# Performance work log

Hardware: AMD Instinct MI355X
Metric: run time of the kernel (lower is better)

The kernel has to match this reference:

```python
import jax, jax.numpy as jnp
import numpy as np

N_NODES = 50000
N_EDGES = 800000
D_FEAT = 128
HIDDEN = 256
N_CLASSES = 2


def setup_inputs() -> dict:
    key = jax.random.key(0)
    ks = jax.random.split(key, 9)
    x = jax.random.normal(ks[0], (N_NODES, D_FEAT), dtype=jnp.float32)
    edge_index = jax.random.randint(ks[1], (2, N_EDGES), 0, N_NODES, dtype=jnp.int32)
    # SAGEConv params: lin_l (applied to aggregated neighbors), lin_r (root), bias
    s1 = 1.0 / np.sqrt(D_FEAT)
    s2 = 1.0 / np.sqrt(HIDDEN)
    W1l = jax.random.normal(ks[2], (D_FEAT, HIDDEN), dtype=jnp.float32) * s1
    W1r = jax.random.normal(ks[3], (D_FEAT, HIDDEN), dtype=jnp.float32) * s1
    b1 = jax.random.normal(ks[4], (HIDDEN,), dtype=jnp.float32) * s1
    W2l = jax.random.normal(ks[5], (HIDDEN, N_CLASSES), dtype=jnp.float32) * s2
    W2r = jax.random.normal(ks[6], (HIDDEN, N_CLASSES), dtype=jnp.float32) * s2
    b2 = jax.random.normal(ks[7], (N_CLASSES,), dtype=jnp.float32) * s2
    return {"x": x, "edge_index": edge_index, "W1l": W1l, "W1r": W1r,
            "b1": b1, "W2l": W2l, "W2r": W2r, "b2": b2}


def _sage_conv(x, src, dst, Wl, Wr, b):
    # mean-aggregate neighbor features x[src] into destination nodes
    n = x.shape[0]
    agg = jax.ops.segment_sum(x[src], dst, num_segments=n)  # [N, d]
    deg = jax.ops.segment_sum(jnp.ones((src.shape[0],), x.dtype), dst,
                              num_segments=n)
    mean = agg / jnp.maximum(deg, 1.0)[:, None]
    return mean @ Wl + x @ Wr + b


def reference(x, edge_index, W1l, W1r, b1, W2l, W2r, b2):
    src, dst = edge_index[0], edge_index[1]
    h = jax.nn.relu(_sage_conv(x, src, dst, W1l, W1r, b1))
    embeddings = h  # dropout is identity in eval mode
    out = jax.nn.sigmoid(_sage_conv(embeddings, src, dst, W2l, W2r, b2))
    return out, embeddings
```

## Files before the change

kernel.cpp:

```cpp
#include <hip/hip_runtime.h>
#include <math.h>

#define N_NODES 50000
#define N_EDGES 800000
#define D_FEAT 128
#define HIDDEN 256
#define NB_SCAN 196
#define GEMM_BLOCKS 1563

#define AGG_B 2048

#define CVT_B 512
#define CNT_B 3125
#define CP_B (CVT_B + CNT_B)
#define SCAT_B 3125

typedef __bf16 bf16x8 __attribute__((ext_vector_type(8)));
typedef float f32x4 __attribute__((ext_vector_type(4)));

__device__ __forceinline__ unsigned f2b(float f) {
    unsigned u = __builtin_bit_cast(unsigned, f);
    return (u + 0x7fff + ((u >> 16) & 1)) >> 16;
}

__global__ __launch_bounds__(256) void count_prep(
    const float* __restrict__ x, const int* __restrict__ dst,
    const float* __restrict__ W1l, const float* __restrict__ W1r,
    int* __restrict__ cnt, unsigned short* __restrict__ rank,
    unsigned* __restrict__ xb, unsigned short* __restrict__ Wfrag) {
    int b = blockIdx.x;
    int t = threadIdx.x;
    if (b < CVT_B) {
        for (int g = b * 256 + t; g < 800000; g += CVT_B * 256) {
            float4 v0 = *(const float4*)(x + (size_t)g * 8);
            float4 v1 = *(const float4*)(x + (size_t)g * 8 + 4);
            uint4 o;
            o.x = f2b(v0.x) | (f2b(v0.y) << 16);
            o.y = f2b(v0.z) | (f2b(v0.w) << 16);
            o.z = f2b(v1.x) | (f2b(v1.y) << 16);
            o.w = f2b(v1.z) | (f2b(v1.w) << 16);
            int d = g >> 4;
            int j = (g & 15) << 2;
            *(uint4*)(xb + (size_t)d * 64 + j) = o;
        }
        for (int tt = b * 256 + t; tt < 65536; tt += CVT_B * 256) {
            int j = tt & 7;
            int lane = (tt >> 3) & 63;
            int ks = (tt >> 9) & 7;
            int nt = tt >> 12;
            int k = ks * 32 + ((lane >> 4) << 3) + j;
            int n = (nt << 4) + (lane & 15);
            float v = (k < 128) ? W1l[k * 256 + n] : W1r[(k - 128) * 256 + n];
            Wfrag[tt] = (unsigned short)f2b(v);
        }
    } else {
        int e = (b - CVT_B) * 256 + t;
        if (e < N_EDGES) {
            int d = dst[e];
            rank[e] = (unsigned short)atomicAdd(&cnt[d], 1);
        }
    }
}

__global__ void scan1(const int* __restrict__ cnt, int* __restrict__ bsum) {
    __shared__ int tmp[256];
    int t = threadIdx.x;
    int i = blockIdx.x * 256 + t;
    int c = (i < N_NODES) ? cnt[i] : 0;
    tmp[t] = c;
    __syncthreads();
    for (int off = 128; off > 0; off >>= 1) {
        if (t < off) tmp[t] += tmp[t + off];
        __syncthreads();
    }
    if (t == 0) bsum[blockIdx.x] = tmp[0];
}

__global__ void scanB(const int* __restrict__ cnt, const int* __restrict__ bsum,
                      int* __restrict__ rowbeg) {
    __shared__ int bs[256];
    __shared__ int tmp[256];
    int t = threadIdx.x;
    int b = blockIdx.x;
    bs[t] = (t < NB_SCAN) ? bsum[t] : 0;
    __syncthreads();
    for (int off = 1; off < 256; off <<= 1) {
        int y = (t >= off) ? bs[t - off] : 0;
        __syncthreads();
        bs[t] += y;
        __syncthreads();
    }
    int boff = (b == 0) ? 0 : bs[b - 1];
    int i = b * 256 + t;
    int v = (i < N_NODES) ? cnt[i] : 0;
    tmp[t] = v;
    __syncthreads();
    for (int off = 1; off < 256; off <<= 1) {
        int y = (t >= off) ? tmp[t - off] : 0;
        __syncthreads();
        tmp[t] += y;
        __syncthreads();
    }
    if (i < N_NODES) rowbeg[i] = tmp[t] - v + boff;
}

__global__ __launch_bounds__(256) void scatter2(
    const int* __restrict__ src, const int* __restrict__ dst,
    const int* __restrict__ rowbeg, const unsigned short* __restrict__ rank,
    unsigned short* __restrict__ esrc) {
    int e = blockIdx.x * 256 + threadIdx.x;
    if (e < N_EDGES) {
        int d = dst[e];
        unsigned pos = (unsigned)rowbeg[d] + (unsigned)rank[e];
        esrc[pos] = (unsigned short)src[e];
    }
}

__global__ __launch_bounds__(256) void agg1(
    const unsigned* __restrict__ xb, unsigned* __restrict__ mb,
    const unsigned short* __restrict__ esrc,
    const int* __restrict__ rowbeg, const int* __restrict__ cnt) {
    int wid = (blockIdx.x * 256 + threadIdx.x) >> 6;
    int lane = threadIdx.x & 63;
    int g = lane >> 4;
    int i = lane & 15;
    for (int d = wid; d < N_NODES; d += AGG_B * 4) {
        int beg = rowbeg[d];
        int c = cnt[d];
        int end = beg + c;
        float acc[8];
#pragma unroll
        for (int f = 0; f < 8; f++) acc[f] = 0.0f;

        for (int base = beg; base < end; base += 64) {
            int m = end - base; if (m > 64) m = 64;
            int idx = base + lane;
            int e = (int)esrc[idx < end ? idx : end - 1];
            for (int j0 = 0; j0 < m; j0 += 4) {
                int ss = __shfl(e, j0 + g);
                float sc = (j0 + g < m) ? 1.0f : 0.0f;
                uint4 u = *(const uint4*)(xb + (size_t)ss * 64 + (i << 2));
                acc[0] += sc * __builtin_bit_cast(float, u.x << 16);
                acc[1] += sc * __builtin_bit_cast(float, u.x & 0xffff0000u);
                acc[2] += sc * __builtin_bit_cast(float, u.y << 16);
                acc[3] += sc * __builtin_bit_cast(float, u.y & 0xffff0000u);
                acc[4] += sc * __builtin_bit_cast(float, u.z << 16);
                acc[5] += sc * __builtin_bit_cast(float, u.z & 0xffff0000u);
                acc[6] += sc * __builtin_bit_cast(float, u.w << 16);
                acc[7] += sc * __builtin_bit_cast(float, u.w & 0xffff0000u);
            }
        }
#pragma unroll
        for (int f = 0; f < 8; f++) {
            acc[f] += __shfl_xor(acc[f], 16);
            acc[f] += __shfl_xor(acc[f], 32);
        }
        if (lane < 16) {
            float inv = 1.0f / fmaxf((float)c, 1.0f);
            uint4 o;
            o.x = f2b(acc[0] * inv) | (f2b(acc[1] * inv) << 16);
            o.y = f2b(acc[2] * inv) | (f2b(acc[3] * inv) << 16);
            o.z = f2b(acc[4] * inv) | (f2b(acc[5] * inv) << 16);
            o.w = f2b(acc[6] * inv) | (f2b(acc[7] * inv) << 16);
            *(uint4*)(mb + (size_t)d * 64 + (i << 2)) = o;
        }
    }
}

__global__ __launch_bounds__(256) void gemm1ps(
    const unsigned* __restrict__ mb, const unsigned* __restrict__ xb,
    const unsigned short* __restrict__ Wfrag, const float* __restrict__ b1,
    const float* __restrict__ W2l, const float* __restrict__ W2r,
    const float* __restrict__ b2,
    float* __restrict__ h, float* __restrict__ p, float* __restrict__ s) {
    __shared__ union {
        unsigned A[32 * 128];
        float H[16 * 260];
    } sm;
    __shared__ float ppart[32][4];

    int r0 = blockIdx.x * 32;
    int tid = threadIdx.x;
    int w = tid >> 6;
    int lane = tid & 63;
    int quad = lane >> 4;
    int l15 = lane & 15;

    if (tid < 128) ((float*)ppart)[tid] = 0.0f;

    int sr = tid >> 3;
    int c0 = tid & 7;
#pragma unroll
    for (int j = 0; j < 4; j++) {
        int c = c0 + (j << 3);
        uint4 v;
        if (c < 16) v = *(const uint4*)(mb + (size_t)(r0 + sr) * 64 + (c << 2));
        else        v = *(const uint4*)(xb + (size_t)(r0 + sr) * 64 + ((c - 16) << 2));
        int cp = c ^ (sr & 7);
        *(uint4*)(sm.A + sr * 128 + (cp << 2)) = v;
    }
    __syncthreads();

    f32x4 acc[8];
#pragma unroll
    for (int i = 0; i < 8; i++) acc[i] = (f32x4){0.0f, 0.0f, 0.0f, 0.0f};

    for (int ks = 0; ks < 8; ks++) {
        bf16x8 bfr[4];
#pragma unroll
        for (int nt = 0; nt < 4; nt++) {
            int ntg = (w << 2) + nt;
            uint4 raw = *(const uint4*)(Wfrag + ((((ntg << 3) + ks) << 6) + lane) * 8);
            bfr[nt] = __builtin_bit_cast(bf16x8, raw);
        }
#pragma unroll
        for (int mt = 0; mt < 2; mt++) {
            int row = (mt << 4) + l15;
            int c = (ks << 2) + quad;
            uint4 araw = *(const uint4*)(sm.A + row * 128 + ((c ^ (row & 7)) << 2));
            bf16x8 afr = __builtin_bit_cast(bf16x8, araw);
#pragma unroll
            for (int nt = 0; nt < 4; nt++) {
                acc[(mt << 2) + nt] = __builtin_amdgcn_mfma_f32_16x16x32_bf16(
                    afr, bfr[nt], acc[(mt << 2) + nt], 0, 0, 0);
            }
        }
    }

    float w2[4][4];
#pragma unroll
    for (int nt = 0; nt < 4; nt++) {
        int col = (w << 6) + (nt << 4) + l15;
        float2 l2 = *(const float2*)(W2l + col * 2);
        float2 r2 = *(const float2*)(W2r + col * 2);
        w2[nt][0] = l2.x; w2[nt][1] = l2.y; w2[nt][2] = r2.x; w2[nt][3] = r2.y;
    }

#pragma unroll
    for (int mt = 0; mt < 2; mt++) {
        __syncthreads();
        float red[4][4];
#pragma unroll
        for (int v = 0; v < 4; v++)
#pragma unroll
            for (int r = 0; r < 4; r++) red[v][r] = 0.0f;

#pragma unroll
        for (int nt = 0; nt < 4; nt++) {
            int col = (w << 6) + (nt << 4) + l15;
            float b = b1[col];
            f32x4 v = acc[(mt << 2) + nt];
#pragma unroll
            for (int r = 0; r < 4; r++) {
                float hv = v[r] + b;
                hv = hv > 0.0f ? hv : 0.0f;
                int lrow = (quad << 2) + r;
                sm.H[lrow * 260 + col] = hv;
                red[0][r] += hv * w2[nt][0];
                red[1][r] += hv * w2[nt][1];
                red[2][r] += hv * w2[nt][2];
                red[3][r] += hv * w2[nt][3];
            }
        }
#pragma unroll
        for (int v = 0; v < 4; v++)
#pragma unroll
            for (int r = 0; r < 4; r++) {
                red[v][r] += __shfl_xor(red[v][r], 1);
                red[v][r] += __shfl_xor(red[v][r], 2);
                red[v][r] += __shfl_xor(red[v][r], 4);
                red[v][r] += __shfl_xor(red[v][r], 8);
            }
        if (l15 == 0) {
            int lrow = (mt << 4) + (quad << 2);
#pragma unroll
            for (int r = 0; r < 4; r++)
#pragma unroll
                for (int v = 0; v < 4; v++)
                    atomicAdd(&ppart[lrow + r][v], red[v][r]);
        }
        __syncthreads();
        int rg0 = r0 + (mt << 4);
#pragma unroll
        for (int k = 0; k < 4; k++) {
            int lr = (k << 2) + w;
            int row = rg0 + lr;
            if (row < N_NODES) {
                f32x4 v4 = *(const f32x4*)(sm.H + lr * 260 + (lane << 2));
                __builtin_nontemporal_store(
                    v4, (f32x4*)(h + (size_t)row * 256 + (lane << 2)));
            }
        }
    }

    if (tid < 32) {
        int row = r0 + tid;
        if (row < N_NODES) {
            float2 pv = {ppart[tid][0], ppart[tid][1]};
            float2 sv = {ppart[tid][2] + b2[0], ppart[tid][3] + b2[1]};
            *(float2*)(p + (size_t)row * 2) = pv;
            *(float2*)(s + (size_t)row * 2) = sv;
        }
    }
}

__global__ __launch_bounds__(256) void agg2(
    const float* __restrict__ p, const float* __restrict__ s,
    const unsigned short* __restrict__ esrc,
    const int* __restrict__ rowbeg, const int* __restrict__ cnt,
    float* __restrict__ out) {
    int wid = (blockIdx.x * 256 + threadIdx.x) >> 6;
    int lane = threadIdx.x & 63;
    for (int d = wid; d < N_NODES; d += AGG_B * 4) {
        int beg = rowbeg[d];
        int c = cnt[d];
        int end = beg + c;
        float a0 = 0.0f, a1 = 0.0f;
        for (int base = beg; base < end; base += 64) {
            int idx = base + lane;
            if (idx < end) {
                int ss = (int)esrc[idx];
                float2 v = *(const float2*)(p + (size_t)ss * 2);
                a0 += v.x; a1 += v.y;
            }
        }
#pragma unroll
        for (int off = 32; off > 0; off >>= 1) {
            a0 += __shfl_down(a0, off);
            a1 += __shfl_down(a1, off);
        }
        if (lane == 0) {
            float inv = 1.0f / fmaxf((float)c, 1.0f);
            float z0 = a0 * inv + s[(size_t)d * 2 + 0];
            float z1 = a1 * inv + s[(size_t)d * 2 + 1];
            float2 o = {1.0f / (1.0f + expf(-z0)), 1.0f / (1.0f + expf(-z1))};
            *(float2*)(out + (size_t)d * 2) = o;
        }
    }
}

extern "C" void kernel_launch(void* const* d_in, const int* in_sizes, int n_in,
                              void* d_out, int out_size, void* d_ws, size_t ws_size,
                              hipStream_t stream) {
    const float* x   = (const float*)d_in[0];
    const int*   ei  = (const int*)d_in[1];
    const float* W1l = (const float*)d_in[2];
    const float* W1r = (const float*)d_in[3];
    const float* b1  = (const float*)d_in[4];
    const float* W2l = (const float*)d_in[5];
    const float* W2r = (const float*)d_in[6];
    const float* b2  = (const float*)d_in[7];

    const int* src = ei;
    const int* dst = ei + N_EDGES;

    float* out = (float*)d_out;
    float* emb = out + (size_t)N_NODES * 2;

    int* cnt    = (int*)d_ws;
    int* rowbeg = cnt + N_NODES;
    int* bsum   = rowbeg + N_NODES;
    unsigned short* esrc = (unsigned short*)(bsum + 256);
    unsigned* xb = (unsigned*)(esrc + 800064);
    unsigned* mb = xb + (size_t)50048 * 64;
    unsigned short* Wfrag = (unsigned short*)(mb + (size_t)50048 * 64);
    float* p = (float*)(Wfrag + 65536);
    float* s = p + (size_t)N_NODES * 2;
    unsigned short* rank = (unsigned short*)emb;

    (void)hipMemsetAsync(cnt, 0, N_NODES * sizeof(int), stream);

    count_prep<<<CP_B, 256, 0, stream>>>(x, dst, W1l, W1r, cnt, rank, xb, Wfrag);
    scan1<<<NB_SCAN, 256, 0, stream>>>(cnt, bsum);
    scanB<<<NB_SCAN, 256, 0, stream>>>(cnt, bsum, rowbeg);
    scatter2<<<SCAT_B, 256, 0, stream>>>(src, dst, rowbeg, rank, esrc);

    agg1<<<AGG_B, 256, 0, stream>>>(xb, mb, esrc, rowbeg, cnt);

    gemm1ps<<<GEMM_BLOCKS, 256, 0, stream>>>(mb, xb, Wfrag, b1, W2l, W2r, b2,
                                             emb, p, s);

    agg2<<<AGG_B, 256, 0, stream>>>(p, s, esrc, rowbeg, cnt, out);
}
```

Measured before the change: 217.5 us.

## Fuse first-layer neighbor aggregation into the GEMM kernel via shared memory

Removes the separate agg1 kernel and the mb intermediate buffer. Each GEMM block now computes the mean-aggregated neighbor rows for its 32 nodes directly into the swizzled shared-memory A tile, with each wave handling 8 rows. The gather loop is also software-pipelined to issue the next neighbor load before accumulating the current one, and launch bounds request 4 blocks per CU. This saves a kernel launch and the global write and re-read of the aggregated features. The cost is that aggregation load imbalance from varying degrees now stalls the GEMM blocks, and only 4 waves per block do the gather.

Result: slower. 229.3 us (+5.4%).

```diff
diff --git a/kernel.cpp b/kernel.cpp
--- a/kernel.cpp
+++ b/kernel.cpp
@@ -22,6 +22,16 @@
     unsigned u = __builtin_bit_cast(unsigned, f);
     return (u + 0x7fff + ((u >> 16) & 1)) >> 16;
 }
+
+#define ACC8(U, SC)                                                     \
+    acc[0] += (SC) * __builtin_bit_cast(float, (U).x << 16);            \
+    acc[1] += (SC) * __builtin_bit_cast(float, (U).x & 0xffff0000u);    \
+    acc[2] += (SC) * __builtin_bit_cast(float, (U).y << 16);            \
+    acc[3] += (SC) * __builtin_bit_cast(float, (U).y & 0xffff0000u);    \
+    acc[4] += (SC) * __builtin_bit_cast(float, (U).z << 16);            \
+    acc[5] += (SC) * __builtin_bit_cast(float, (U).z & 0xffff0000u);    \
+    acc[6] += (SC) * __builtin_bit_cast(float, (U).w << 16);            \
+    acc[7] += (SC) * __builtin_bit_cast(float, (U).w & 0xffff0000u);
 
 __global__ __launch_bounds__(256) void count_prep(
     const float* __restrict__ x, const int* __restrict__ dst,
@@ -116,59 +126,9 @@
     }
 }
 
-__global__ __launch_bounds__(256) void agg1(
-    const unsigned* __restrict__ xb, unsigned* __restrict__ mb,
-    const unsigned short* __restrict__ esrc,
-    const int* __restrict__ rowbeg, const int* __restrict__ cnt) {
-    int wid = (blockIdx.x * 256 + threadIdx.x) >> 6;
-    int lane = threadIdx.x & 63;
-    int g = lane >> 4;
-    int i = lane & 15;
-    for (int d = wid; d < N_NODES; d += AGG_B * 4) {
-        int beg = rowbeg[d];
-        int c = cnt[d];
-        int end = beg + c;
-        float acc[8];
-#pragma unroll
-        for (int f = 0; f < 8; f++) acc[f] = 0.0f;
-
-        for (int base = beg; base < end; base += 64) {
-            int m = end - base; if (m > 64) m = 64;
-            int idx = base + lane;
-            int e = (int)esrc[idx < end ? idx : end - 1];
-            for (int j0 = 0; j0 < m; j0 += 4) {
-                int ss = __shfl(e, j0 + g);
-                float sc = (j0 + g < m) ? 1.0f : 0.0f;
-                uint4 u = *(const uint4*)(xb + (size_t)ss * 64 + (i << 2));
-                acc[0] += sc * __builtin_bit_cast(float, u.x << 16);
-                acc[1] += sc * __builtin_bit_cast(float, u.x & 0xffff0000u);
-                acc[2] += sc * __builtin_bit_cast(float, u.y << 16);
-                acc[3] += sc * __builtin_bit_cast(float, u.y & 0xffff0000u);
-                acc[4] += sc * __builtin_bit_cast(float, u.z << 16);
-                acc[5] += sc * __builtin_bit_cast(float, u.z & 0xffff0000u);
-                acc[6] += sc * __builtin_bit_cast(float, u.w << 16);
-                acc[7] += sc * __builtin_bit_cast(float, u.w & 0xffff0000u);
-            }
-        }
-#pragma unroll
-        for (int f = 0; f < 8; f++) {
-            acc[f] += __shfl_xor(acc[f], 16);
-            acc[f] += __shfl_xor(acc[f], 32);
-        }
-        if (lane < 16) {
-            float inv = 1.0f / fmaxf((float)c, 1.0f);
-            uint4 o;
-            o.x = f2b(acc[0] * inv) | (f2b(acc[1] * inv) << 16);
-            o.y = f2b(acc[2] * inv) | (f2b(acc[3] * inv) << 16);
-            o.z = f2b(acc[4] * inv) | (f2b(acc[5] * inv) << 16);
-            o.w = f2b(acc[6] * inv) | (f2b(acc[7] * inv) << 16);
-            *(uint4*)(mb + (size_t)d * 64 + (i << 2)) = o;
-        }
-    }
-}
-
-__global__ __launch_bounds__(256) void gemm1ps(
-    const unsigned* __restrict__ mb, const unsigned* __restrict__ xb,
+__global__ __launch_bounds__(256, 4) void agg_gemm(
+    const unsigned* __restrict__ xb, const unsigned short* __restrict__ esrc,
+    const int* __restrict__ rowbeg, const int* __restrict__ cnt,
     const unsigned short* __restrict__ Wfrag, const float* __restrict__ b1,
     const float* __restrict__ W2l, const float* __restrict__ W2r,
     const float* __restrict__ b2,
@@ -188,16 +148,65 @@
 
     if (tid < 128) ((float*)ppart)[tid] = 0.0f;
 
-    int sr = tid >> 3;
-    int c0 = tid & 7;
-#pragma unroll
-    for (int j = 0; j < 4; j++) {
-        int c = c0 + (j << 3);
-        uint4 v;
-        if (c < 16) v = *(const uint4*)(mb + (size_t)(r0 + sr) * 64 + (c << 2));
-        else        v = *(const uint4*)(xb + (size_t)(r0 + sr) * 64 + ((c - 16) << 2));
-        int cp = c ^ (sr & 7);
-        *(uint4*)(sm.A + sr * 128 + (cp << 2)) = v;
+    {
+        int sr = tid >> 3;
+        int c0 = tid & 7;
+#pragma unroll
+        for (int j = 2; j < 4; j++) {
+            int c = c0 + (j << 3);
+            uint4 v = *(const uint4*)(xb + (size_t)(r0 + sr) * 64 + ((c - 16) << 2));
+            int cp = c ^ (sr & 7);
+            *(uint4*)(sm.A + sr * 128 + (cp << 2)) = v;
+        }
+    }
+
+    {
+        int g4 = lane >> 4;
+        int i4 = lane & 15;
+#pragma unroll 1
+        for (int k = 0; k < 8; k++) {
+            int lrow = (w << 3) + k;
+            int d = r0 + lrow;
+            if (d >= N_NODES) break;
+            int beg = rowbeg[d];
+            int c = cnt[d];
+            int end = beg + c;
+            float acc[8];
+#pragma unroll
+            for (int f = 0; f < 8; f++) acc[f] = 0.0f;
+
+            for (int base = beg; base < end; base += 64) {
+                int m = end - base; if (m > 64) m = 64;
+                int idx = base + lane;
+                int e = (int)esrc[idx < end ? idx : end - 1];
+                int ss = __shfl(e, g4);
+                float sc = (g4 < m) ? 1.0f : 0.0f;
+                uint4 u = *(const uint4*)(xb + (size_t)ss * 64 + (i4 << 2));
+                for (int j0 = 4; j0 < m; j0 += 4) {
+                    int ssn = __shfl(e, j0 + g4);
+                    float scn = (j0 + g4 < m) ? 1.0f : 0.0f;
+                    uint4 un = *(const uint4*)(xb + (size_t)ssn * 64 + (i4 << 2));
+                    ACC8(u, sc)
+                    u = un;
+                    sc = scn;
+                }
+                ACC8(u, sc)
+            }
+#pragma unroll
+            for (int f = 0; f < 8; f++) {
+                acc[f] += __shfl_xor(acc[f], 16);
+                acc[f] += __shfl_xor(acc[f], 32);
+            }
+            if (lane < 16) {
+                float inv = 1.0f / fmaxf((float)c, 1.0f);
+                uint4 o;
+                o.x = f2b(acc[0] * inv) | (f2b(acc[1] * inv) << 16);
+                o.y = f2b(acc[2] * inv) | (f2b(acc[3] * inv) << 16);
+                o.z = f2b(acc[4] * inv) | (f2b(acc[5] * inv) << 16);
+                o.w = f2b(acc[6] * inv) | (f2b(acc[7] * inv) << 16);
+                *(uint4*)(sm.A + lrow * 128 + ((i4 ^ (lrow & 7)) << 2)) = o;
+            }
+        }
     }
     __syncthreads();
 
@@ -362,8 +371,7 @@
     int* bsum   = rowbeg + N_NODES;
     unsigned short* esrc = (unsigned short*)(bsum + 256);
     unsigned* xb = (unsigned*)(esrc + 800064);
-    unsigned* mb = xb + (size_t)50048 * 64;
-    unsigned short* Wfrag = (unsigned short*)(mb + (size_t)50048 * 64);
+    unsigned short* Wfrag = (unsigned short*)(xb + (size_t)50048 * 64);
     float* p = (float*)(Wfrag + 65536);
     float* s = p + (size_t)N_NODES * 2;
     unsigned short* rank = (unsigned short*)emb;
@@ -375,10 +383,8 @@
     scanB<<<NB_SCAN, 256, 0, stream>>>(cnt, bsum, rowbeg);
     scatter2<<<SCAT_B, 256, 0, stream>>>(src, dst, rowbeg, rank, esrc);
 
-    agg1<<<AGG_B, 256, 0, stream>>>(xb, mb, esrc, rowbeg, cnt);
-
-    gemm1ps<<<GEMM_BLOCKS, 256, 0, stream>>>(mb, xb, Wfrag, b1, W2l, W2r, b2,
-                                             emb, p, s);
+    agg_gemm<<<GEMM_BLOCKS, 256, 0, stream>>>(xb, esrc, rowbeg, cnt, Wfrag,
+                                              b1, W2l, W2r, b2, emb, p, s);
 
     agg2<<<AGG_B, 256, 0, stream>>>(p, s, esrc, rowbeg, cnt, out);
 }
```
